# Performance work log

Measured on AMD Instinct MI355X. Metric: run time of the kernel, lower is better.

Reference implementation:

```python
import jax, jax.numpy as jnp
import numpy as np

B, T, C = 2, 2048, 1024
H = 16
D = C // H
STRIDE = 2
EPS = 1e-5


def _strided_allowed(T, stride):
    # position i attends to j if j<=i and (j >= i-4 local band OR j % stride == 0)
    i = jnp.arange(T)[:, None]
    j = jnp.arange(T)[None, :]
    return (j <= i) & ((j >= i - 4) | (j % stride == 0))


def _layernorm(x, w, b):
    mu = jnp.mean(x, axis=-1, keepdims=True)
    var = jnp.mean(jnp.square(x - mu), axis=-1, keepdims=True)
    return (x - mu) * jax.lax.rsqrt(var + EPS) * w + b


def setup_inputs() -> dict:
    key = jax.random.key(0)
    ks = jax.random.split(key, 8)
    s = 0.02
    return {
        "x": jax.random.normal(ks[0], (B, T, C), dtype=jnp.float32),
        "ln1_w": jnp.ones((C,), jnp.float32),
        "ln1_b": jnp.zeros((C,), jnp.float32),
        "c_attn_w": s * jax.random.normal(ks[1], (C, 3 * C), jnp.float32),  # [in,out]
        "c_attn_b": jnp.zeros((3 * C,), jnp.float32),
        "attn_proj_w": s * jax.random.normal(ks[2], (C, C), jnp.float32),
        "attn_proj_b": jnp.zeros((C,), jnp.float32),
        "ln2_w": jnp.ones((C,), jnp.float32),
        "ln2_b": jnp.zeros((C,), jnp.float32),
        "fc_w": s * jax.random.normal(ks[3], (C, 4 * C), jnp.float32),
        "fc_b": jnp.zeros((4 * C,), jnp.float32),
        "mlp_proj_w": s * jax.random.normal(ks[4], (4 * C, C), jnp.float32),
        "mlp_proj_b": jnp.zeros((C,), jnp.float32),
    }


def reference(x, ln1_w, ln1_b, c_attn_w, c_attn_b, attn_proj_w, attn_proj_b,
              ln2_w, ln2_b, fc_w, fc_b, mlp_proj_w, mlp_proj_b):
    Bx, Tx, Cx = x.shape
    # --- sparse (strided) causal attention on ln_1(x) ---
    h = _layernorm(x, ln1_w, ln1_b)
    qkv = h @ c_attn_w + c_attn_b                      # [B,T,3C]
    q, k, v = jnp.split(qkv, 3, axis=-1)
    q = q.reshape(Bx, Tx, H, D).transpose(0, 2, 1, 3)  # [B,H,T,D]
    k = k.reshape(Bx, Tx, H, D).transpose(0, 2, 1, 3)
    v = v.reshape(Bx, Tx, H, D).transpose(0, 2, 1, 3)
    scale = 1.0 / np.sqrt(D)
    att = jnp.einsum('bhqd,bhkd->bhqk', q, k) * scale  # dense [B,H,T,T] as in source
    allowed = _strided_allowed(Tx, STRIDE)             # [T,T] bool
    att = jnp.where(allowed[None, None], att, -jnp.inf)
    att = jax.nn.softmax(att, axis=-1)
    y = jnp.einsum('bhqk,bhkd->bhqd', att, v)
    y = y.transpose(0, 2, 1, 3).reshape(Bx, Tx, Cx)
    y = y @ attn_proj_w + attn_proj_b
    x = x + y
    # --- MLP on ln_2(x) ---
    h2 = _layernorm(x, ln2_w, ln2_b)
    h2 = jax.nn.gelu(h2 @ fc_w + fc_b, approximate=False)
    x = x + (h2 @ mlp_proj_w + mlp_proj_b)
    return x
```

## Files before the change

### kernel.cpp

```cpp
#include <hip/hip_runtime.h>
#include <hip/hip_bf16.h>

#define Bn 2
#define Tn 2048
#define Cn 1024
#define Hn 16
#define Dn 64
#define Mrows (Bn * Tn)

typedef __attribute__((ext_vector_type(8))) short short8;
typedef __attribute__((ext_vector_type(4))) float f32x4;

typedef const __attribute__((address_space(1))) unsigned int* gas_ptr;
typedef __attribute__((address_space(3))) unsigned int* las_ptr;

__device__ __forceinline__ unsigned short f2b(float f) {
  unsigned int u = __builtin_bit_cast(unsigned int, f);
  return (unsigned short)((u + 0x7fffu + ((u >> 16) & 1u)) >> 16);
}

__device__ __forceinline__ float gelu_f(float v) {
  float u2 = v + 0.044715f * v * v * v;
  float e = __expf(1.5957691216f * u2);
  float th = 1.0f - 2.0f / (e + 1.0f);
  return 0.5f * v * (1.0f + th);
}

__device__ __forceinline__ void ln_row(const float* __restrict__ x, const float* __restrict__ w,
                                       const float* __restrict__ b, unsigned short* __restrict__ out,
                                       int row, float* ls, float* ls2) {
  const int t = threadIdx.x;
  const float4 v = *reinterpret_cast<const float4*>(x + (size_t)row * Cn + t * 4);
  float s = v.x + v.y + v.z + v.w;
  float s2 = v.x * v.x + v.y * v.y + v.z * v.z + v.w * v.w;
#pragma unroll
  for (int m = 1; m < 64; m <<= 1) { s += __shfl_xor(s, m); s2 += __shfl_xor(s2, m); }
  if ((t & 63) == 0) { ls[t >> 6] = s; ls2[t >> 6] = s2; }
  __syncthreads();
  s  = ls[0] + ls[1] + ls[2] + ls[3];
  s2 = ls2[0] + ls2[1] + ls2[2] + ls2[3];
  const float mu = s * (1.0f / Cn);
  const float rstd = rsqrtf(s2 * (1.0f / Cn) - mu * mu + 1e-5f);
  const float4 wv = *reinterpret_cast<const float4*>(w + t * 4);
  const float4 bv = *reinterpret_cast<const float4*>(b + t * 4);
  unsigned short o[4];
  o[0] = f2b((v.x - mu) * rstd * wv.x + bv.x);
  o[1] = f2b((v.y - mu) * rstd * wv.y + bv.y);
  o[2] = f2b((v.z - mu) * rstd * wv.z + bv.z);
  o[3] = f2b((v.w - mu) * rstd * wv.w + bv.w);
  *reinterpret_cast<uint2*>(out + (size_t)row * Cn + t * 4) = *reinterpret_cast<uint2*>(o);
}

__global__ __launch_bounds__(256) void ln_kernel(const float* __restrict__ x,
                                                 const float* __restrict__ w,
                                                 const float* __restrict__ b,
                                                 unsigned short* __restrict__ out) {
  __shared__ float ls[4], ls2[4];
  ln_row(x, w, b, out, blockIdx.x, ls, ls2);
}

__global__ __launch_bounds__(256) void prep_kernel(
    const float* __restrict__ W0, unsigned short* __restrict__ T0,
    const float* __restrict__ W1, unsigned short* __restrict__ T1,
    const float* __restrict__ W2, unsigned short* __restrict__ T2,
    const float* __restrict__ W3, unsigned short* __restrict__ T3,
    const float* __restrict__ x, const float* __restrict__ ln1w,
    const float* __restrict__ ln1b, unsigned short* __restrict__ h) {
  __shared__ float tile[32][33];
  __shared__ float ls[4], ls2[4];
  int b = blockIdx.x;
  if (b >= 12288) {
    ln_row(x, ln1w, ln1b, h, b - 12288, ls, ls2);
    return;
  }
  const float* W; unsigned short* T; int K, N;
  if (b < 3072)      { W = W0; T = T0; K = 1024; N = 3072; }
  else if (b < 4096) { W = W1; T = T1; K = 1024; N = 1024; b -= 3072; }
  else if (b < 8192) { W = W2; T = T2; K = 1024; N = 4096; b -= 4096; }
  else               { W = W3; T = T3; K = 4096; N = 1024; b -= 8192; }
  const int nx = N >> 5;
  const int n0 = (b % nx) * 32, k0 = (b / nx) * 32;
  const int tx = threadIdx.x & 31, ty = threadIdx.x >> 5;
#pragma unroll
  for (int r = 0; r < 4; r++)
    tile[ty + r * 8][tx] = W[(size_t)(k0 + ty + r * 8) * N + n0 + tx];
  __syncthreads();
#pragma unroll
  for (int r = 0; r < 4; r++)
    T[(size_t)(n0 + ty + r * 8) * K + k0 + tx] = f2b(tile[tx][ty + r * 8]);
}

#define BUFS 16384
template <int EP>
__global__ __launch_bounds__(512, 2) void gemm256_kernel(
    const unsigned short* __restrict__ A, const unsigned short* __restrict__ Bt,
    const float* __restrict__ bias, void* out, int M, int N, int K, int nx) {
  extern __shared__ unsigned short lds[];
  const int tid = threadIdx.x;
  const int lane = tid & 63, w = tid >> 6;
  const int wm = w >> 2, wn = w & 3;
  const int l15 = lane & 15, l4 = lane >> 4;

  const int nwg = gridDim.x;
  int wg = blockIdx.x;
  wg = (wg & 7) * (nwg >> 3) + (wg >> 3);
  const int tile_m = (wg / nx) * 256;
  const int tile_n = (wg % nx) * 256;

  f32x4 acc[8][4] = {};

  const int ch0 = w * 64 + lane;
  const int r0 = ch0 >> 2;
  const int c0 = (((ch0 & 3) ^ ((r0 >> 1) & 3))) * 8;
  const unsigned short* gA0 = A + (size_t)(tile_m + r0) * K + c0;
  const unsigned short* gA1 = gA0 + (size_t)128 * K;
  const unsigned short* gB0 = Bt + (size_t)(tile_n + r0) * K + c0;
  const unsigned short* gB1 = gB0 + (size_t)128 * K;
  const int ldsA0 = (w * 64) * 8, ldsA1 = (512 + w * 64) * 8;

  auto stage = [&](unsigned short* Ab, int t) {
    unsigned short* Bb = Ab + 8192;
    const size_t ko = (size_t)t * 32;
    __builtin_amdgcn_global_load_lds((gas_ptr)(gA0 + ko), (las_ptr)&Ab[ldsA0], 16, 0, 0);
    __builtin_amdgcn_global_load_lds((gas_ptr)(gA1 + ko), (las_ptr)&Ab[ldsA1], 16, 0, 0);
    __builtin_amdgcn_global_load_lds((gas_ptr)(gB0 + ko), (las_ptr)&Bb[ldsA0], 16, 0, 0);
    __builtin_amdgcn_global_load_lds((gas_ptr)(gB1 + ko), (las_ptr)&Bb[ldsA1], 16, 0, 0);
  };

  stage(lds, 0);
  stage(lds + BUFS, 1);
  stage(lds + 2 * BUFS, 2);
  asm volatile("s_waitcnt vmcnt(8)" ::: "memory");
  __builtin_amdgcn_s_barrier();
  __builtin_amdgcn_sched_barrier(0);

  const int ca = (l4 ^ ((l15 >> 1) & 3)) * 8;

  const int nt = K >> 5;
  for (int tb = 0; tb < nt; tb += 4) {
#pragma unroll
    for (int u = 0; u < 4; u++) {
      const int t = tb + u;
      if (t + 3 < nt) stage(lds + (((u + 3) & 3) * BUFS), t + 3);

      const unsigned short* Ab = lds + u * BUFS;
      const unsigned short* Bb = Ab + 8192;
      short8 a[4], b[4], a2[4];
#pragma unroll
      for (int i = 0; i < 4; i++) {
        a[i] = *reinterpret_cast<const short8*>(&Ab[(wm * 128 + i * 16 + l15) * 32 + ca]);
        b[i] = *reinterpret_cast<const short8*>(&Bb[(wn * 64 + i * 16 + l15) * 32 + ca]);
      }
      __builtin_amdgcn_sched_barrier(0);
#pragma unroll
      for (int i = 0; i < 4; i++)
        a2[i] = *reinterpret_cast<const short8*>(&Ab[(wm * 128 + 64 + i * 16 + l15) * 32 + ca]);

      asm volatile("s_waitcnt lgkmcnt(4)" ::: "memory");
      __builtin_amdgcn_sched_barrier(0);
      __builtin_amdgcn_s_setprio(1);
#pragma unroll
      for (int mi = 0; mi < 4; mi++)
#pragma unroll
        for (int ni = 0; ni < 4; ni++)
          acc[mi][ni] = __builtin_amdgcn_mfma_f32_16x16x32_bf16(a[mi], b[ni], acc[mi][ni], 0, 0, 0);
      __builtin_amdgcn_s_setprio(0);
      __builtin_amdgcn_sched_barrier(0);

      asm volatile("s_waitcnt lgkmcnt(0)" ::: "memory");
      __builtin_amdgcn_sched_barrier(0);
      __builtin_amdgcn_s_setprio(1);
#pragma unroll
      for (int mi = 0; mi < 4; mi++)
#pragma unroll
        for (int ni = 0; ni < 4; ni++)
          acc[mi + 4][ni] = __builtin_amdgcn_mfma_f32_16x16x32_bf16(a2[mi], b[ni], acc[mi + 4][ni], 0, 0, 0);
      __builtin_amdgcn_s_setprio(0);
      __builtin_amdgcn_sched_barrier(0);

      if (t + 3 < nt) {
        asm volatile("s_waitcnt vmcnt(8)" ::: "memory");
      } else if (t + 2 < nt) {
        asm volatile("s_waitcnt vmcnt(4)" ::: "memory");
      } else if (t + 1 < nt) {
        asm volatile("s_waitcnt vmcnt(0)" ::: "memory");
      }
      __builtin_amdgcn_s_barrier();
      __builtin_amdgcn_sched_barrier(0);
    }
  }

#pragma unroll
  for (int ni = 0; ni < 4; ni++) {
    const int col = tile_n + wn * 64 + ni * 16 + l15;
    const float bv = bias[col];
#pragma unroll
    for (int mi = 0; mi < 8; mi++) {
#pragma unroll
      for (int r = 0; r < 4; r++) {
        const int row = tile_m + wm * 128 + mi * 16 + l4 * 4 + r;
        const size_t idx = (size_t)row * N + col;
        float v = acc[mi][ni][r] + bv;
        if (EP == 0) {
          ((unsigned short*)out)[idx] = f2b(v);
        } else {
          ((unsigned short*)out)[idx] = f2b(gelu_f(v));
        }
      }
    }
  }
}

__global__ __launch_bounds__(512, 1) void gemm128_kernel(
    const unsigned short* __restrict__ A, const unsigned short* __restrict__ Bt,
    const float* __restrict__ bias, const float* __restrict__ res, float* __restrict__ out,
    int M, int N, int K, int nx) {
  extern __shared__ unsigned short lds[];
  const int tid = threadIdx.x;
  const int lane = tid & 63, w = tid >> 6;
  const int wm = w >> 2, wn = w & 3;
  const int l15 = lane & 15, l4 = lane >> 4;

  const int nwg = gridDim.x;
  int wg = blockIdx.x;
  wg = (wg & 7) * (nwg >> 3) + (wg >> 3);
  const int tile_m = (wg / nx) * 128;
  const int tile_n = (wg % nx) * 128;

  f32x4 acc[4][2] = {};

  const unsigned short* Gs = (w < 4) ? A : Bt;
  const int tb0 = (w < 4) ? tile_m : tile_n;
  const int ch0 = (w & 3) * 128 + lane;
  const int r0c = ch0 >> 2;
  const int c0s = (((ch0 & 3) ^ ((r0c >> 1) & 3))) * 8;
  const unsigned short* g0 = Gs + (size_t)(tb0 + r0c) * K + c0s;
  const unsigned short* g1 = g0 + (size_t)16 * K;
  const int lds0 = ((w & 3) * 128) * 8, lds1 = ((w & 3) * 128 + 64) * 8;
  const int half = (w < 4) ? 0 : 4096;

  auto stage = [&](int slot, int t) {
    unsigned short* Lb = lds + slot * 8192 + half;
    const size_t ko = (size_t)t * 32;
    __builtin_amdgcn_global_load_lds((gas_ptr)(g0 + ko), (las_ptr)&Lb[lds0], 16, 0, 0);
    __builtin_amdgcn_global_load_lds((gas_ptr)(g1 + ko), (las_ptr)&Lb[lds1], 16, 0, 0);
  };

  stage(0, 0);
  stage(1, 1);
  stage(2, 2);
  stage(3, 3);
  asm volatile("s_waitcnt vmcnt(4)" ::: "memory");
  __builtin_amdgcn_s_barrier();
  __builtin_amdgcn_sched_barrier(0);

  const int ca = (l4 ^ ((l15 >> 1) & 3)) * 8;

  const int nt = K >> 5;
  const int np = nt >> 1;
  for (int p = 0; p < np; ++p) {
    const int t0 = 2 * p;
    if (t0 + 4 < nt) stage((t0 + 4) % 6, t0 + 4);
    if (t0 + 5 < nt) stage((t0 + 5) % 6, t0 + 5);

    const unsigned short* A0 = lds + (t0 % 6) * 8192;
    const unsigned short* B0 = A0 + 4096;
    const unsigned short* A1 = lds + ((t0 + 1) % 6) * 8192;
    const unsigned short* B1 = A1 + 4096;
    short8 a[2], b[2], a2[2], c[2], d[2], c2[2];
#pragma unroll
    for (int i = 0; i < 2; i++) {
      a[i] = *reinterpret_cast<const short8*>(&A0[(wm * 64 + i * 16 + l15) * 32 + ca]);
      b[i] = *reinterpret_cast<const short8*>(&B0[(wn * 32 + i * 16 + l15) * 32 + ca]);
    }
    __builtin_amdgcn_sched_barrier(0);
#pragma unroll
    for (int i = 0; i < 2; i++)
      a2[i] = *reinterpret_cast<const short8*>(&A0[(wm * 64 + 32 + i * 16 + l15) * 32 + ca]);
    __builtin_amdgcn_sched_barrier(0);
#pragma unroll
    for (int i = 0; i < 2; i++) {
      c[i] = *reinterpret_cast<const short8*>(&A1[(wm * 64 + i * 16 + l15) * 32 + ca]);
      d[i] = *reinterpret_cast<const short8*>(&B1[(wn * 32 + i * 16 + l15) * 32 + ca]);
    }
    __builtin_amdgcn_sched_barrier(0);
#pragma unroll
    for (int i = 0; i < 2; i++)
      c2[i] = *reinterpret_cast<const short8*>(&A1[(wm * 64 + 32 + i * 16 + l15) * 32 + ca]);

    asm volatile("s_waitcnt lgkmcnt(8)" ::: "memory");
    __builtin_amdgcn_sched_barrier(0);
    __builtin_amdgcn_s_setprio(1);
#pragma unroll
    for (int mi = 0; mi < 2; mi++)
#pragma unroll
      for (int ni = 0; ni < 2; ni++)
        acc[mi][ni] = __builtin_amdgcn_mfma_f32_16x16x32_bf16(a[mi], b[ni], acc[mi][ni], 0, 0, 0);
    __builtin_amdgcn_s_setprio(0);
    __builtin_amdgcn_sched_barrier(0);

    asm volatile("s_waitcnt lgkmcnt(6)" ::: "memory");
    __builtin_amdgcn_sched_barrier(0);
    __builtin_amdgcn_s_setprio(1);
#pragma unroll
    for (int mi = 0; mi < 2; mi++)
#pragma unroll
      for (int ni = 0; ni < 2; ni++)
        acc[mi + 2][ni] = __builtin_amdgcn_mfma_f32_16x16x32_bf16(a2[mi], b[ni], acc[mi + 2][ni], 0, 0, 0);
    __builtin_amdgcn_s_setprio(0);
    __builtin_amdgcn_sched_barrier(0);

    asm volatile("s_waitcnt lgkmcnt(2)" ::: "memory");
    __builtin_amdgcn_sched_barrier(0);
    __builtin_amdgcn_s_setprio(1);
#pragma unroll
    for (int mi = 0; mi < 2; mi++)
#pragma unroll
      for (int ni = 0; ni < 2; ni++)
        acc[mi][ni] = __builtin_amdgcn_mfma_f32_16x16x32_bf16(c[mi], d[ni], acc[mi][ni], 0, 0, 0);
    __builtin_amdgcn_s_setprio(0);
    __builtin_amdgcn_sched_barrier(0);

    asm volatile("s_waitcnt lgkmcnt(0)" ::: "memory");
    __builtin_amdgcn_sched_barrier(0);
    __builtin_amdgcn_s_setprio(1);
#pragma unroll
    for (int mi = 0; mi < 2; mi++)
#pragma unroll
      for (int ni = 0; ni < 2; ni++)
        acc[mi + 2][ni] = __builtin_amdgcn_mfma_f32_16x16x32_bf16(c2[mi], d[ni], acc[mi + 2][ni], 0, 0, 0);
    __builtin_amdgcn_s_setprio(0);
    __builtin_amdgcn_sched_barrier(0);

    if (t0 + 4 < nt) {
      asm volatile("s_waitcnt vmcnt(4)" ::: "memory");
    } else if (t0 + 2 < nt) {
      asm volatile("s_waitcnt vmcnt(0)" ::: "memory");
    }
    __builtin_amdgcn_s_barrier();
    __builtin_amdgcn_sched_barrier(0);
  }

#pragma unroll
  for (int ni = 0; ni < 2; ni++) {
    const int col = tile_n + wn * 32 + ni * 16 + l15;
    const float bv = bias[col];
#pragma unroll
    for (int mi = 0; mi < 4; mi++) {
#pragma unroll
      for (int r = 0; r < 4; r++) {
        const int row = tile_m + wm * 64 + mi * 16 + l4 * 4 + r;
        const size_t idx = (size_t)row * N + col;
        out[idx] = acc[mi][ni][r] + bv + res[idx];
      }
    }
  }
}

__global__ __launch_bounds__(256, 4) void attn_kernel(const unsigned short* __restrict__ qkv,
                                                      unsigned short* __restrict__ y) {
  __shared__ unsigned short SH[17408];
  const int tid = threadIdx.x;
  const int lane = tid & 63, w = tid >> 6;
  const int l15 = lane & 15, l4 = lane >> 4;

  const int bi = blockIdx.x;
  const int quarter = bi >> 8, rest = bi & 255;
  const int bh = rest >> 3, sub = rest & 7;
  int qt;
  if (quarter == 0) qt = sub;
  else if (quarter == 1) qt = 15 - sub;
  else if (quarter == 2) qt = 16 + sub;
  else qt = 31 - sub;
  const int bb = bh >> 4, hh = bh & 15;
  const int q0 = qt * 64;
  const size_t base = (size_t)bb * Tn * (3 * Cn) + hh * 64;

  const int nfar = qt >> 1;
  const int ntiles = nfar + (q0 ? 2 : 1);

  unsigned short* Vt = SH + 8192;
  unsigned short* Ps = SH + 12800 + w * 1152;

  auto keyof = [&](int t, int row) -> int {
    if (t < nfar) return t * 128 + 2 * row;
    return q0 - 64 * (ntiles - 1 - t) + row;
  };
  auto stageK = [&](int t) {
    unsigned short* kb = SH + ((t & 1) << 12);
#pragma unroll
    for (int u = 0; u < 2; u++) {
      const int chunk = u * 256 + tid;
      const int row = chunk >> 3, cc = chunk & 7;
      const int csrc = cc ^ (row & 7);
      const int key = keyof(t, row);
      __builtin_amdgcn_global_load_lds(
          (gas_ptr)&qkv[base + Cn + (size_t)key * (3 * Cn) + csrc * 8],
          (las_ptr)&kb[(u * 256 + (w << 6)) * 8], 16, 0, 0);
    }
  };
  uint4 vr[2];
  auto fetchV = [&](int t) {
#pragma unroll
    for (int u = 0; u < 2; u++) {
      const int chunk = u * 256 + tid;
      const int row = chunk >> 3, cc = chunk & 7;
      const int key = keyof(t, row);
      vr[u] = *reinterpret_cast<const uint4*>(&qkv[base + 2 * Cn + (size_t)key * (3 * Cn) + cc * 8]);
    }
  };

#pragma unroll
  for (int u = 0; u < 2; u++) {
    const int chunk = u * 256 + tid;
    const int row = chunk >> 3, cc = chunk & 7;
    const int csrc = cc ^ (row & 7);
    __builtin_amdgcn_global_load_lds(
        (gas_ptr)&qkv[base + (size_t)(q0 + row) * (3 * Cn) + csrc * 8],
        (las_ptr)&SH[(u * 256 + (w << 6)) * 8], 16, 0, 0);
  }
  __syncthreads();
  short8 qf[2];
#pragma unroll
  for (int ks = 0; ks < 2; ks++) {
    const int r = (w << 4) + l15;
    qf[ks] = *reinterpret_cast<const short8*>(&SH[r * 64 + (((ks * 4 + l4) ^ (l15 & 7)) * 8)]);
  }
  asm volatile("s_waitcnt lgkmcnt(0)" ::: "memory");
  __builtin_amdgcn_s_barrier();
  __builtin_amdgcn_sched_barrier(0);
  stageK(0);
  fetchV(0);
  __syncthreads();

  f32x4 acc_o[4] = {};
  float mrow[4], lrow[4];
#pragma unroll
  for (int r = 0; r < 4; r++) { mrow[r] = -1e30f; lrow[r] = 0.0f; }

  for (int t = 0; t < ntiles; ++t) {
#pragma unroll
    for (int u = 0; u < 2; u++) {
      const int chunk = u * 256 + tid;
      const int row = chunk >> 3, cc = chunk & 7;
      unsigned short tmp[8];
      *reinterpret_cast<uint4*>(tmp) = vr[u];
      const int xr = row ^ (cc << 3);
#pragma unroll
      for (int j = 0; j < 8; j++) Vt[(cc * 8 + j) * 72 + xr] = tmp[j];
    }
    if (t + 1 < ntiles) { stageK(t + 1); fetchV(t + 1); }
    asm volatile("s_waitcnt lgkmcnt(0)" ::: "memory");
    __builtin_amdgcn_s_barrier();
    __builtin_amdgcn_sched_barrier(0);

    const unsigned short* Kb = SH + ((t & 1) << 12);
    f32x4 s[4] = {};
#pragma unroll
    for (int ni = 0; ni < 4; ni++) {
#pragma unroll
      for (int ks = 0; ks < 2; ks++) {
        const int r = ni * 16 + l15;
        short8 kf = *reinterpret_cast<const short8*>(&Kb[r * 64 + (((ks * 4 + l4) ^ (l15 & 7)) * 8)]);
        s[ni] = __builtin_amdgcn_mfma_f32_16x16x32_bf16(qf[ks], kf, s[ni], 0, 0, 0);
      }
    }

    const bool far = (t < nfar);
    const int kb0 = far ? t * 128 : q0 - 64 * (ntiles - 1 - t);
#pragma unroll
    for (int ni = 0; ni < 4; ni++) {
      const int pos = ni * 16 + l15;
      const int j = far ? kb0 + 2 * pos : kb0 + pos;
#pragma unroll
      for (int r = 0; r < 4; r++) {
        float v = s[ni][r] * 0.125f;
        if (far) {
          v = (j < q0 - 64) ? v : -1e30f;
        } else {
          const int iq = q0 + (w << 4) + l4 * 4 + r;
          const bool ok = (j <= iq) && ((j >= iq - 4) || ((j & 1) == 0));
          v = ok ? v : -1e30f;
        }
        s[ni][r] = v;
      }
    }

    float tmx[4];
    bool need = false;
#pragma unroll
    for (int r = 0; r < 4; r++) {
      float tm = fmaxf(fmaxf(s[0][r], s[1][r]), fmaxf(s[2][r], s[3][r]));
      tm = fmaxf(tm, __shfl_xor(tm, 1));
      tm = fmaxf(tm, __shfl_xor(tm, 2));
      tm = fmaxf(tm, __shfl_xor(tm, 4));
      tm = fmaxf(tm, __shfl_xor(tm, 8));
      tmx[r] = tm;
      need = need || (tm > mrow[r] + 8.0f);
    }
    if (__any(need)) {
#pragma unroll
      for (int r = 0; r < 4; r++) {
        const float mnew = fmaxf(mrow[r], tmx[r]);
        const float alpha = __expf(mrow[r] - mnew);
        mrow[r] = mnew;
        lrow[r] *= alpha;
#pragma unroll
        for (int nd = 0; nd < 4; nd++) acc_o[nd][r] *= alpha;
      }
    }
#pragma unroll
    for (int r = 0; r < 4; r++) {
      float rs = 0.0f;
#pragma unroll
      for (int ni = 0; ni < 4; ni++) {
        const float pv = __expf(s[ni][r] - mrow[r]);
        s[ni][r] = pv;
        rs += pv;
      }
      rs += __shfl_xor(rs, 1); rs += __shfl_xor(rs, 2);
      rs += __shfl_xor(rs, 4); rs += __shfl_xor(rs, 8);
      lrow[r] += rs;
    }

#pragma unroll
    for (int ni = 0; ni < 4; ni++)
#pragma unroll
      for (int r = 0; r < 4; r++)
        Ps[(l4 * 4 + r) * 72 + ni * 16 + l15] = f2b(s[ni][r]);

#pragma unroll
    for (int kss = 0; kss < 2; kss++) {
      short8 pf = *reinterpret_cast<const short8*>(&Ps[l15 * 72 + kss * 32 + l4 * 8]);
#pragma unroll
      for (int nd = 0; nd < 4; nd++) {
        const int d = nd * 16 + l15;
        const int kcol = (kss * 32 + l4 * 8) ^ ((d >> 3) << 3);
        short8 vf = *reinterpret_cast<const short8*>(&Vt[d * 72 + kcol]);
        acc_o[nd] = __builtin_amdgcn_mfma_f32_16x16x32_bf16(pf, vf, acc_o[nd], 0, 0, 0);
      }
    }

    __syncthreads();
  }

#pragma unroll
  for (int r = 0; r < 4; r++) {
    const float inv = 1.0f / lrow[r];
    const int row = q0 + (w << 4) + l4 * 4 + r;
#pragma unroll
    for (int nd = 0; nd < 4; nd++) {
      const int col = nd * 16 + l15;
      y[((size_t)bb * Tn + row) * Cn + hh * 64 + col] = f2b(acc_o[nd][r] * inv);
    }
  }
}

extern "C" void kernel_launch(void* const* d_in, const int* in_sizes, int n_in,
                              void* d_out, int out_size, void* d_ws, size_t ws_size,
                              hipStream_t stream) {
  const float* x           = (const float*)d_in[0];
  const float* ln1_w       = (const float*)d_in[1];
  const float* ln1_b       = (const float*)d_in[2];
  const float* c_attn_w    = (const float*)d_in[3];
  const float* c_attn_b    = (const float*)d_in[4];
  const float* attn_proj_w = (const float*)d_in[5];
  const float* attn_proj_b = (const float*)d_in[6];
  const float* ln2_w       = (const float*)d_in[7];
  const float* ln2_b       = (const float*)d_in[8];
  const float* fc_w        = (const float*)d_in[9];
  const float* fc_b        = (const float*)d_in[10];
  const float* mlp_proj_w  = (const float*)d_in[11];
  const float* mlp_proj_b  = (const float*)d_in[12];
  float* out = (float*)d_out;

  char* ws = (char*)d_ws;
  unsigned short* wT1 = (unsigned short*)(ws);
  unsigned short* wT2 = (unsigned short*)(ws + 6291456);
  unsigned short* wT3 = (unsigned short*)(ws + 8388608);
  unsigned short* wT4 = (unsigned short*)(ws + 16777216);
  unsigned short* h   = (unsigned short*)(ws + 25165824);
  unsigned short* qkv = (unsigned short*)(ws + 33554432);
  unsigned short* yb  = (unsigned short*)(ws + 67108864);

  hipFuncSetAttribute((const void*)gemm256_kernel<0>, hipFuncAttributeMaxDynamicSharedMemorySize, 131072);
  hipFuncSetAttribute((const void*)gemm256_kernel<2>, hipFuncAttributeMaxDynamicSharedMemorySize, 131072);
  hipFuncSetAttribute((const void*)gemm128_kernel, hipFuncAttributeMaxDynamicSharedMemorySize, 98304);

  prep_kernel<<<16384, 256, 0, stream>>>(c_attn_w, wT1, attn_proj_w, wT2,
                                         fc_w, wT3, mlp_proj_w, wT4,
                                         x, ln1_w, ln1_b, h);
  gemm256_kernel<0><<<(Mrows / 256) * (3072 / 256), 512, 131072, stream>>>(
      h, wT1, c_attn_b, qkv, Mrows, 3072, 1024, 3072 / 256);
  attn_kernel<<<1024, 256, 0, stream>>>(qkv, yb);
  gemm128_kernel<<<(Mrows / 128) * (1024 / 128), 512, 98304, stream>>>(
      yb, wT2, attn_proj_b, x, out, Mrows, 1024, 1024, 1024 / 128);
  ln_kernel<<<Mrows, 256, 0, stream>>>(out, ln2_w, ln2_b, h);
  gemm256_kernel<2><<<(Mrows / 256) * (4096 / 256), 512, 131072, stream>>>(
      h, wT3, fc_b, qkv, Mrows, 4096, 1024, 4096 / 256);
  gemm128_kernel<<<(Mrows / 128) * (1024 / 128), 512, 98304, stream>>>(
      qkv, wT4, mlp_proj_b, out, out, Mrows, 1024, 4096, 1024 / 128);
}
```

Before: 221.4 us.

## Interleave GEMM prefetch loads with MFMA clusters in finer-grained phases

```diff
diff --git a/kernel.cpp b/kernel.cpp
--- a/kernel.cpp
+++ b/kernel.cpp
@@ -92,7 +92,7 @@
 
 #define BUFS 16384
 template <int EP>
-__global__ __launch_bounds__(512, 2) void gemm256_kernel(
+__global__ __launch_bounds__(512, 1) void gemm256_kernel(
     const unsigned short* __restrict__ A, const unsigned short* __restrict__ Bt,
     const float* __restrict__ bias, void* out, int M, int N, int K, int nx) {
   extern __shared__ unsigned short lds[];
@@ -118,18 +118,22 @@
   const unsigned short* gB1 = gB0 + (size_t)128 * K;
   const int ldsA0 = (w * 64) * 8, ldsA1 = (512 + w * 64) * 8;
 
-  auto stage = [&](unsigned short* Ab, int t) {
+  auto stage1 = [&](int slot, int t, int j) {
+    unsigned short* Ab = lds + slot * BUFS;
     unsigned short* Bb = Ab + 8192;
     const size_t ko = (size_t)t * 32;
-    __builtin_amdgcn_global_load_lds((gas_ptr)(gA0 + ko), (las_ptr)&Ab[ldsA0], 16, 0, 0);
-    __builtin_amdgcn_global_load_lds((gas_ptr)(gA1 + ko), (las_ptr)&Ab[ldsA1], 16, 0, 0);
-    __builtin_amdgcn_global_load_lds((gas_ptr)(gB0 + ko), (las_ptr)&Bb[ldsA0], 16, 0, 0);
-    __builtin_amdgcn_global_load_lds((gas_ptr)(gB1 + ko), (las_ptr)&Bb[ldsA1], 16, 0, 0);
+    if (j == 0)      __builtin_amdgcn_global_load_lds((gas_ptr)(gA0 + ko), (las_ptr)&Ab[ldsA0], 16, 0, 0);
+    else if (j == 1) __builtin_amdgcn_global_load_lds((gas_ptr)(gA1 + ko), (las_ptr)&Ab[ldsA1], 16, 0, 0);
+    else if (j == 2) __builtin_amdgcn_global_load_lds((gas_ptr)(gB0 + ko), (las_ptr)&Bb[ldsA0], 16, 0, 0);
+    else             __builtin_amdgcn_global_load_lds((gas_ptr)(gB1 + ko), (las_ptr)&Bb[ldsA1], 16, 0, 0);
   };
-
-  stage(lds, 0);
-  stage(lds + BUFS, 1);
-  stage(lds + 2 * BUFS, 2);
+  auto stage4 = [&](int slot, int t) {
+    stage1(slot, t, 0); stage1(slot, t, 1); stage1(slot, t, 2); stage1(slot, t, 3);
+  };
+
+  stage4(0, 0);
+  stage4(1, 1);
+  stage4(2, 2);
   asm volatile("s_waitcnt vmcnt(8)" ::: "memory");
   __builtin_amdgcn_s_barrier();
   __builtin_amdgcn_sched_barrier(0);
@@ -137,53 +141,50 @@
   const int ca = (l4 ^ ((l15 >> 1) & 3)) * 8;
 
   const int nt = K >> 5;
-  for (int tb = 0; tb < nt; tb += 4) {
-#pragma unroll
-    for (int u = 0; u < 4; u++) {
-      const int t = tb + u;
-      if (t + 3 < nt) stage(lds + (((u + 3) & 3) * BUFS), t + 3);
-
-      const unsigned short* Ab = lds + u * BUFS;
+  for (int t = 0; t < nt; t += 2) {
+    short8 b[4];
+#pragma unroll
+    for (int q = 0; q < 8; q++) {
+      const int half = q >> 2;
+      const int c = q & 3;
+      const int ss = (t + half) & 3;
+      const unsigned short* Ab = lds + ss * BUFS;
       const unsigned short* Bb = Ab + 8192;
-      short8 a[4], b[4], a2[4];
-#pragma unroll
-      for (int i = 0; i < 4; i++) {
-        a[i] = *reinterpret_cast<const short8*>(&Ab[(wm * 128 + i * 16 + l15) * 32 + ca]);
-        b[i] = *reinterpret_cast<const short8*>(&Bb[(wn * 64 + i * 16 + l15) * 32 + ca]);
-      }
+
+      const int st = t + 3 + half;
+      if (st < nt) stage1(st & 3, st, c);
+
+      if (c == 0) {
+#pragma unroll
+        for (int i = 0; i < 4; i++)
+          b[i] = *reinterpret_cast<const short8*>(&Bb[(wn * 64 + i * 16 + l15) * 32 + ca]);
+      }
+      short8 a0 = *reinterpret_cast<const short8*>(&Ab[(wm * 128 + c * 32 + l15) * 32 + ca]);
+      short8 a1 = *reinterpret_cast<const short8*>(&Ab[(wm * 128 + c * 32 + 16 + l15) * 32 + ca]);
       __builtin_amdgcn_sched_barrier(0);
-#pragma unroll
-      for (int i = 0; i < 4; i++)
-        a2[i] = *reinterpret_cast<const short8*>(&Ab[(wm * 128 + 64 + i * 16 + l15) * 32 + ca]);
-
-      asm volatile("s_waitcnt lgkmcnt(4)" ::: "memory");
-      __builtin_amdgcn_sched_barrier(0);
-      __builtin_amdgcn_s_setprio(1);
-#pragma unroll
-      for (int mi = 0; mi < 4; mi++)
-#pragma unroll
-        for (int ni = 0; ni < 4; ni++)
-          acc[mi][ni] = __builtin_amdgcn_mfma_f32_16x16x32_bf16(a[mi], b[ni], acc[mi][ni], 0, 0, 0);
-      __builtin_amdgcn_s_setprio(0);
-      __builtin_amdgcn_sched_barrier(0);
-
+
+      __builtin_amdgcn_s_barrier();
       asm volatile("s_waitcnt lgkmcnt(0)" ::: "memory");
       __builtin_amdgcn_sched_barrier(0);
       __builtin_amdgcn_s_setprio(1);
 #pragma unroll
-      for (int mi = 0; mi < 4; mi++)
-#pragma unroll
-        for (int ni = 0; ni < 4; ni++)
-          acc[mi + 4][ni] = __builtin_amdgcn_mfma_f32_16x16x32_bf16(a2[mi], b[ni], acc[mi + 4][ni], 0, 0, 0);
+      for (int ni = 0; ni < 4; ni++) {
+        acc[c * 2][ni]     = __builtin_amdgcn_mfma_f32_16x16x32_bf16(a0, b[ni], acc[c * 2][ni], 0, 0, 0);
+        acc[c * 2 + 1][ni] = __builtin_amdgcn_mfma_f32_16x16x32_bf16(a1, b[ni], acc[c * 2 + 1][ni], 0, 0, 0);
+      }
       __builtin_amdgcn_s_setprio(0);
       __builtin_amdgcn_sched_barrier(0);
 
-      if (t + 3 < nt) {
-        asm volatile("s_waitcnt vmcnt(8)" ::: "memory");
-      } else if (t + 2 < nt) {
-        asm volatile("s_waitcnt vmcnt(4)" ::: "memory");
-      } else if (t + 1 < nt) {
-        asm volatile("s_waitcnt vmcnt(0)" ::: "memory");
+      if (c == 3) {
+        if (half == 0) {
+          if (t + 3 < nt)      asm volatile("s_waitcnt vmcnt(8)" ::: "memory");
+          else if (t + 2 < nt) asm volatile("s_waitcnt vmcnt(4)" ::: "memory");
+          else                 asm volatile("s_waitcnt vmcnt(0)" ::: "memory");
+        } else if (t + 2 < nt) {
+          if (t + 4 < nt)      asm volatile("s_waitcnt vmcnt(8)" ::: "memory");
+          else if (t + 3 < nt) asm volatile("s_waitcnt vmcnt(4)" ::: "memory");
+          else                 asm volatile("s_waitcnt vmcnt(0)" ::: "memory");
+        }
       }
       __builtin_amdgcn_s_barrier();
       __builtin_amdgcn_sched_barrier(0);
```

After: 228.7 us. 3.3% more time.

## Give each attention wave its own head and full query tile

Applied to the files above, without the earlier changes.

```diff
diff --git a/kernel.cpp b/kernel.cpp
--- a/kernel.cpp
+++ b/kernel.cpp
@@ -357,21 +357,18 @@
   }
 }
 
-__global__ __launch_bounds__(256, 4) void attn_kernel(const unsigned short* __restrict__ qkv,
+__global__ __launch_bounds__(256, 2) void attn_kernel(const unsigned short* __restrict__ qkv,
                                                       unsigned short* __restrict__ y) {
-  __shared__ unsigned short SH[17408];
+  extern __shared__ unsigned short AS[];
   const int tid = threadIdx.x;
   const int lane = tid & 63, w = tid >> 6;
   const int l15 = lane & 15, l4 = lane >> 4;
 
   const int bi = blockIdx.x;
-  const int quarter = bi >> 8, rest = bi & 255;
-  const int bh = rest >> 3, sub = rest & 7;
-  int qt;
-  if (quarter == 0) qt = sub;
-  else if (quarter == 1) qt = 15 - sub;
-  else if (quarter == 2) qt = 16 + sub;
-  else qt = 31 - sub;
+  int qt, bhg;
+  if (bi < 256) { qt = bi >> 3; bhg = bi & 7; }
+  else { const int rr = bi - 256; qt = 31 - (rr >> 3); bhg = rr & 7; }
+  const int bh = bhg * 4 + w;
   const int bb = bh >> 4, hh = bh & 15;
   const int q0 = qt * 64;
   const size_t base = (size_t)bb * Tn * (3 * Cn) + hh * 64;
@@ -379,181 +376,187 @@
   const int nfar = qt >> 1;
   const int ntiles = nfar + (q0 ? 2 : 1);
 
-  unsigned short* Vt = SH + 8192;
-  unsigned short* Ps = SH + 12800 + w * 1152;
+  unsigned short* Kb = AS + w * 9856;
+  unsigned short* Vt = Kb + 4096;
+  unsigned short* Ps = Vt + 4608;
 
   auto keyof = [&](int t, int row) -> int {
     if (t < nfar) return t * 128 + 2 * row;
     return q0 - 64 * (ntiles - 1 - t) + row;
   };
   auto stageK = [&](int t) {
-    unsigned short* kb = SH + ((t & 1) << 12);
-#pragma unroll
-    for (int u = 0; u < 2; u++) {
-      const int chunk = u * 256 + tid;
+#pragma unroll
+    for (int j = 0; j < 8; j++) {
+      const int chunk = j * 64 + lane;
       const int row = chunk >> 3, cc = chunk & 7;
       const int csrc = cc ^ (row & 7);
       const int key = keyof(t, row);
       __builtin_amdgcn_global_load_lds(
           (gas_ptr)&qkv[base + Cn + (size_t)key * (3 * Cn) + csrc * 8],
-          (las_ptr)&kb[(u * 256 + (w << 6)) * 8], 16, 0, 0);
+          (las_ptr)&Kb[j * 512], 16, 0, 0);
     }
   };
-  uint4 vr[2];
+  uint4 vr[8];
   auto fetchV = [&](int t) {
 #pragma unroll
-    for (int u = 0; u < 2; u++) {
-      const int chunk = u * 256 + tid;
+    for (int j = 0; j < 8; j++) {
+      const int chunk = j * 64 + lane;
       const int row = chunk >> 3, cc = chunk & 7;
       const int key = keyof(t, row);
-      vr[u] = *reinterpret_cast<const uint4*>(&qkv[base + 2 * Cn + (size_t)key * (3 * Cn) + cc * 8]);
+      vr[j] = *reinterpret_cast<const uint4*>(&qkv[base + 2 * Cn + (size_t)key * (3 * Cn) + cc * 8]);
     }
   };
 
 #pragma unroll
-  for (int u = 0; u < 2; u++) {
-    const int chunk = u * 256 + tid;
+  for (int j = 0; j < 8; j++) {
+    const int chunk = j * 64 + lane;
     const int row = chunk >> 3, cc = chunk & 7;
     const int csrc = cc ^ (row & 7);
     __builtin_amdgcn_global_load_lds(
         (gas_ptr)&qkv[base + (size_t)(q0 + row) * (3 * Cn) + csrc * 8],
-        (las_ptr)&SH[(u * 256 + (w << 6)) * 8], 16, 0, 0);
+        (las_ptr)&Kb[j * 512], 16, 0, 0);
   }
-  __syncthreads();
-  short8 qf[2];
-#pragma unroll
-  for (int ks = 0; ks < 2; ks++) {
-    const int r = (w << 4) + l15;
-    qf[ks] = *reinterpret_cast<const short8*>(&SH[r * 64 + (((ks * 4 + l4) ^ (l15 & 7)) * 8)]);
-  }
+  asm volatile("s_waitcnt vmcnt(0)" ::: "memory");
+  __builtin_amdgcn_sched_barrier(0);
+  short8 qf[4][2];
+#pragma unroll
+  for (int qi = 0; qi < 4; qi++)
+#pragma unroll
+    for (int ks = 0; ks < 2; ks++) {
+      const int r = qi * 16 + l15;
+      qf[qi][ks] = *reinterpret_cast<const short8*>(&Kb[r * 64 + (((ks * 4 + l4) ^ (r & 7)) * 8)]);
+    }
   asm volatile("s_waitcnt lgkmcnt(0)" ::: "memory");
-  __builtin_amdgcn_s_barrier();
   __builtin_amdgcn_sched_barrier(0);
   stageK(0);
   fetchV(0);
-  __syncthreads();
-
-  f32x4 acc_o[4] = {};
-  float mrow[4], lrow[4];
-#pragma unroll
-  for (int r = 0; r < 4; r++) { mrow[r] = -1e30f; lrow[r] = 0.0f; }
+
+  f32x4 acc[4][4] = {};
+  float mrow[4][4], lrow[4][4];
+#pragma unroll
+  for (int qi = 0; qi < 4; qi++)
+#pragma unroll
+    for (int r = 0; r < 4; r++) { mrow[qi][r] = -1e30f; lrow[qi][r] = 0.0f; }
 
   for (int t = 0; t < ntiles; ++t) {
-#pragma unroll
-    for (int u = 0; u < 2; u++) {
-      const int chunk = u * 256 + tid;
+    asm volatile("s_waitcnt vmcnt(8)" ::: "memory");
+    __builtin_amdgcn_sched_barrier(0);
+
+    f32x4 s[4][4] = {};
+#pragma unroll
+    for (int ki = 0; ki < 4; ki++)
+#pragma unroll
+      for (int ks = 0; ks < 2; ks++) {
+        const int r = ki * 16 + l15;
+        short8 kf = *reinterpret_cast<const short8*>(&Kb[r * 64 + (((ks * 4 + l4) ^ (r & 7)) * 8)]);
+#pragma unroll
+        for (int qi = 0; qi < 4; qi++)
+          s[qi][ki] = __builtin_amdgcn_mfma_f32_16x16x32_bf16(qf[qi][ks], kf, s[qi][ki], 0, 0, 0);
+      }
+    __builtin_amdgcn_sched_barrier(0);
+    const int tn = (t + 1 < ntiles) ? t + 1 : t;
+    stageK(tn);
+
+    const bool far = (t < nfar);
+    const int kb0 = far ? t * 128 : q0 - 64 * (ntiles - 1 - t);
+#pragma unroll
+    for (int qi = 0; qi < 4; qi++)
+#pragma unroll
+      for (int ki = 0; ki < 4; ki++) {
+        const int pos = ki * 16 + l15;
+        const int j = far ? kb0 + 2 * pos : kb0 + pos;
+#pragma unroll
+        for (int r = 0; r < 4; r++) {
+          float v = s[qi][ki][r] * 0.125f;
+          if (far) {
+            v = (j < q0 - 64) ? v : -1e30f;
+          } else {
+            const int iq = q0 + qi * 16 + l4 * 4 + r;
+            const bool ok = (j <= iq) && ((j >= iq - 4) || ((j & 1) == 0));
+            v = ok ? v : -1e30f;
+          }
+          s[qi][ki][r] = v;
+        }
+      }
+
+#pragma unroll
+    for (int qi = 0; qi < 4; qi++)
+#pragma unroll
+      for (int r = 0; r < 4; r++) {
+        float tm = fmaxf(fmaxf(s[qi][0][r], s[qi][1][r]), fmaxf(s[qi][2][r], s[qi][3][r]));
+        tm = fmaxf(tm, __shfl_xor(tm, 1));
+        tm = fmaxf(tm, __shfl_xor(tm, 2));
+        tm = fmaxf(tm, __shfl_xor(tm, 4));
+        tm = fmaxf(tm, __shfl_xor(tm, 8));
+        const float mnew = fmaxf(mrow[qi][r], tm);
+        const float alpha = __expf(mrow[qi][r] - mnew);
+        mrow[qi][r] = mnew;
+        lrow[qi][r] *= alpha;
+#pragma unroll
+        for (int nd = 0; nd < 4; nd++) acc[qi][nd][r] *= alpha;
+        float rs = 0.0f;
+#pragma unroll
+        for (int ki = 0; ki < 4; ki++) {
+          const float pv = __expf(s[qi][ki][r] - mnew);
+          s[qi][ki][r] = pv;
+          rs += pv;
+        }
+        rs += __shfl_xor(rs, 1); rs += __shfl_xor(rs, 2);
+        rs += __shfl_xor(rs, 4); rs += __shfl_xor(rs, 8);
+        lrow[qi][r] += rs;
+      }
+
+#pragma unroll
+    for (int j = 0; j < 8; j++) {
+      const int chunk = j * 64 + lane;
       const int row = chunk >> 3, cc = chunk & 7;
       unsigned short tmp[8];
-      *reinterpret_cast<uint4*>(tmp) = vr[u];
+      *reinterpret_cast<uint4*>(tmp) = vr[j];
       const int xr = row ^ (cc << 3);
 #pragma unroll
-      for (int j = 0; j < 8; j++) Vt[(cc * 8 + j) * 72 + xr] = tmp[j];
-    }
-    if (t + 1 < ntiles) { stageK(t + 1); fetchV(t + 1); }
-    asm volatile("s_waitcnt lgkmcnt(0)" ::: "memory");
-    __builtin_amdgcn_s_barrier();
-    __builtin_amdgcn_sched_barrier(0);
-
-    const unsigned short* Kb = SH + ((t & 1) << 12);
-    f32x4 s[4] = {};
-#pragma unroll
-    for (int ni = 0; ni < 4; ni++) {
-#pragma unroll
-      for (int ks = 0; ks < 2; ks++) {
-        const int r = ni * 16 + l15;
-        short8 kf = *reinterpret_cast<const short8*>(&Kb[r * 64 + (((ks * 4 + l4) ^ (l15 & 7)) * 8)]);
-        s[ni] = __builtin_amdgcn_mfma_f32_16x16x32_bf16(qf[ks], kf, s[ni], 0, 0, 0);
-      }
-    }
-
-    const bool far = (t < nfar);
-    const int kb0 = far ? t * 128 : q0 - 64 * (ntiles - 1 - t);
-#pragma unroll
-    for (int ni = 0; ni < 4; ni++) {
-      const int pos = ni * 16 + l15;
-      const int j = far ? kb0 + 2 * pos : kb0 + pos;
-#pragma unroll
-      for (int r = 0; r < 4; r++) {
-        float v = s[ni][r] * 0.125f;
-        if (far) {
-          v = (j < q0 - 64) ? v : -1e30f;
-        } else {
-          const int iq = q0 + (w << 4) + l4 * 4 + r;
-          const bool ok = (j <= iq) && ((j >= iq - 4) || ((j & 1) == 0));
-          v = ok ? v : -1e30f;
-        }
-        s[ni][r] = v;
-      }
-    }
-
-    float tmx[4];
-    bool need = false;
-#pragma unroll
-    for (int r = 0; r < 4; r++) {
-      float tm = fmaxf(fmaxf(s[0][r], s[1][r]), fmaxf(s[2][r], s[3][r]));
-      tm = fmaxf(tm, __shfl_xor(tm, 1));
-      tm = fmaxf(tm, __shfl_xor(tm, 2));
-      tm = fmaxf(tm, __shfl_xor(tm, 4));
-      tm = fmaxf(tm, __shfl_xor(tm, 8));
-      tmx[r] = tm;
-      need = need || (tm > mrow[r] + 8.0f);
-    }
-    if (__any(need)) {
-#pragma unroll
-      for (int r = 0; r < 4; r++) {
-        const float mnew = fmaxf(mrow[r], tmx[r]);
-        const float alpha = __expf(mrow[r] - mnew);
-        mrow[r] = mnew;
-        lrow[r] *= alpha;
-#pragma unroll
-        for (int nd = 0; nd < 4; nd++) acc_o[nd][r] *= alpha;
-      }
-    }
-#pragma unroll
-    for (int r = 0; r < 4; r++) {
-      float rs = 0.0f;
-#pragma unroll
-      for (int ni = 0; ni < 4; ni++) {
-        const float pv = __expf(s[ni][r] - mrow[r]);
-        s[ni][r] = pv;
-        rs += pv;
-      }
-      rs += __shfl_xor(rs, 1); rs += __shfl_xor(rs, 2);
-      rs += __shfl_xor(rs, 4); rs += __shfl_xor(rs, 8);
-      lrow[r] += rs;
-    }
-
-#pragma unroll
-    for (int ni = 0; ni < 4; ni++)
-#pragma unroll
-      for (int r = 0; r < 4; r++)
-        Ps[(l4 * 4 + r) * 72 + ni * 16 + l15] = f2b(s[ni][r]);
-
-#pragma unroll
-    for (int kss = 0; kss < 2; kss++) {
-      short8 pf = *reinterpret_cast<const short8*>(&Ps[l15 * 72 + kss * 32 + l4 * 8]);
-#pragma unroll
-      for (int nd = 0; nd < 4; nd++) {
+      for (int jj = 0; jj < 8; jj++) Vt[(cc * 8 + jj) * 72 + xr] = tmp[jj];
+    }
+    fetchV(tn);
+    __builtin_amdgcn_sched_barrier(0);
+
+    short8 vf[4][2];
+#pragma unroll
+    for (int nd = 0; nd < 4; nd++)
+#pragma unroll
+      for (int kss = 0; kss < 2; kss++) {
         const int d = nd * 16 + l15;
         const int kcol = (kss * 32 + l4 * 8) ^ ((d >> 3) << 3);
-        short8 vf = *reinterpret_cast<const short8*>(&Vt[d * 72 + kcol]);
-        acc_o[nd] = __builtin_amdgcn_mfma_f32_16x16x32_bf16(pf, vf, acc_o[nd], 0, 0, 0);
-      }
-    }
-
-    __syncthreads();
+        vf[nd][kss] = *reinterpret_cast<const short8*>(&Vt[d * 72 + kcol]);
+      }
+#pragma unroll
+    for (int qi = 0; qi < 4; qi++) {
+#pragma unroll
+      for (int ki = 0; ki < 4; ki++)
+#pragma unroll
+        for (int r = 0; r < 4; r++)
+          Ps[(l4 * 4 + r) * 72 + ki * 16 + l15] = f2b(s[qi][ki][r]);
+      short8 pf0 = *reinterpret_cast<const short8*>(&Ps[l15 * 72 + l4 * 8]);
+      short8 pf1 = *reinterpret_cast<const short8*>(&Ps[l15 * 72 + 32 + l4 * 8]);
+#pragma unroll
+      for (int nd = 0; nd < 4; nd++) {
+        acc[qi][nd] = __builtin_amdgcn_mfma_f32_16x16x32_bf16(pf0, vf[nd][0], acc[qi][nd], 0, 0, 0);
+        acc[qi][nd] = __builtin_amdgcn_mfma_f32_16x16x32_bf16(pf1, vf[nd][1], acc[qi][nd], 0, 0, 0);
+      }
+    }
   }
 
 #pragma unroll
-  for (int r = 0; r < 4; r++) {
-    const float inv = 1.0f / lrow[r];
-    const int row = q0 + (w << 4) + l4 * 4 + r;
-#pragma unroll
-    for (int nd = 0; nd < 4; nd++) {
-      const int col = nd * 16 + l15;
-      y[((size_t)bb * Tn + row) * Cn + hh * 64 + col] = f2b(acc_o[nd][r] * inv);
-    }
-  }
+  for (int qi = 0; qi < 4; qi++)
+#pragma unroll
+    for (int r = 0; r < 4; r++) {
+      const float inv = 1.0f / lrow[qi][r];
+      const int row = q0 + qi * 16 + l4 * 4 + r;
+#pragma unroll
+      for (int nd = 0; nd < 4; nd++) {
+        const int col = nd * 16 + l15;
+        y[((size_t)bb * Tn + row) * Cn + hh * 64 + col] = f2b(acc[qi][nd][r] * inv);
+      }
+    }
 }
 
 extern "C" void kernel_launch(void* const* d_in, const int* in_sizes, int n_in,
@@ -586,13 +589,14 @@
   hipFuncSetAttribute((const void*)gemm256_kernel<0>, hipFuncAttributeMaxDynamicSharedMemorySize, 131072);
   hipFuncSetAttribute((const void*)gemm256_kernel<2>, hipFuncAttributeMaxDynamicSharedMemorySize, 131072);
   hipFuncSetAttribute((const void*)gemm128_kernel, hipFuncAttributeMaxDynamicSharedMemorySize, 98304);
+  hipFuncSetAttribute((const void*)attn_kernel, hipFuncAttributeMaxDynamicSharedMemorySize, 78848);
 
   prep_kernel<<<16384, 256, 0, stream>>>(c_attn_w, wT1, attn_proj_w, wT2,
                                          fc_w, wT3, mlp_proj_w, wT4,
                                          x, ln1_w, ln1_b, h);
   gemm256_kernel<0><<<(Mrows / 256) * (3072 / 256), 512, 131072, stream>>>(
       h, wT1, c_attn_b, qkv, Mrows, 3072, 1024, 3072 / 256);
-  attn_kernel<<<1024, 256, 0, stream>>>(qkv, yb);
+  attn_kernel<<<512, 256, 78848, stream>>>(qkv, yb);
   gemm128_kernel<<<(Mrows / 128) * (1024 / 128), 512, 98304, stream>>>(
       yb, wT2, attn_proj_b, x, out, Mrows, 1024, 1024, 1024 / 128);
   ln_kernel<<<Mrows, 256, 0, stream>>>(out, ln2_w, ln2_b, h);
```

New measurement: 408.6 us. 84.5% more time.
